# Optimization experiments

Measured on AMD Instinct MI355X. Metric: run time of the kernel, lower is better.

Reference implementation:

```python
import jax, jax.numpy as jnp
import numpy as np

B, L, D, H = 4, 2048, 256, 512


def silu_backward(x):
    s = jax.nn.silu(x)
    return s + jax.nn.sigmoid(x) * (1.0 - s)


def setup_inputs() -> dict:
    key = jax.random.key(0)
    ks = jax.random.split(key, 12)
    sc = 0.02
    return {
        "x": jax.random.normal(ks[0], (B, L, D), jnp.float32),
        "W1": jax.random.normal(ks[1], (B, H, D), jnp.float32) * sc,
        "W2": jax.random.normal(ks[2], (B, D, H), jnp.float32) * sc,
        "Wq": jax.random.normal(ks[3], (D, D), jnp.float32) * sc,
        "bq": jnp.zeros((D,), jnp.float32),
        "Wk": jax.random.normal(ks[4], (D, D), jnp.float32) * sc,
        "bk": jnp.zeros((D,), jnp.float32),
        "Wv": jax.random.normal(ks[5], (D, D), jnp.float32) * sc,
        "bv": jnp.zeros((D,), jnp.float32),
        "w_lr": jax.random.normal(ks[6], (D,), jnp.float32) * sc,
        "b_lr": jnp.zeros((), jnp.float32),
        "w_wd": jax.random.normal(ks[7], (D,), jnp.float32) * sc,
        "b_wd": jnp.zeros((), jnp.float32),
        "log_base_lr": jnp.asarray(np.log(0.1), jnp.float32),
        "log_base_wd": jnp.asarray(np.log(0.5), jnp.float32),
    }


def reference(x, W1, W2, Wq, bq, Wk, bk, Wv, bv, w_lr, b_lr, w_wd, b_wd, log_base_lr, log_base_wd):
    b, l, d = x.shape
    query = x @ Wq + bq
    key = x @ Wk + bk
    value = x @ Wv + bv
    lr = jnp.exp(log_base_lr) * jax.nn.sigmoid(x @ w_lr + b_lr)          # [b,l]
    log_wd = jnp.log(1.0 - jnp.exp(log_base_wd) * jax.nn.sigmoid(x @ w_wd + b_wd))  # [b,l]

    wd_cross = jnp.exp(jnp.cumsum(log_wd, axis=1))                       # [b,l]
    idx = jnp.arange(l)
    strict_upper = idx[:, None] < idx[None, :]                           # (m, j): j > m
    A = jnp.where(strict_upper[None], log_wd[:, None, :], 0.0)           # [b,m,j]
    wd_inner = jnp.exp(jnp.cumsum(A, axis=2)) * (idx[:, None] <= idx[None, :])[None]  # [b,m,j]

    X1 = key
    Z1 = jnp.einsum('bhd,bld->blh', W1, X1)
    X2 = jax.nn.silu(Z1)
    Z2 = jnp.einsum('bdh,blh->bld', W2, X2)
    grad_Z2 = Z2 - value
    grad_X2 = jnp.einsum('bdh,bld->blh', W2, grad_Z2)
    grad_Z1 = silu_backward(Z1) * grad_X2

    X1_ = query
    mask_X1X1_ = jnp.einsum('bld,bmd->blm', X1, X1_) * wd_inner
    Z1_inner = -jnp.einsum('blh,bl,blm->bmh', grad_Z1, lr, mask_X1X1_)
    Z1_cross = jnp.einsum('bhd,bld,bl->blh', W1, X1_, wd_cross)
    Z1_ = Z1_inner + Z1_cross

    W1_next = (-jnp.einsum('blh,bl,bld->bhd', grad_Z1, lr * wd_inner[:, :, -1], X1)
               + W1 * wd_cross[:, -1][:, None, None])

    X2_ = jax.nn.silu(Z1_)
    mask_X2X2_ = jnp.einsum('blh,bmh->blm', X2, X2_) * wd_inner
    Z2_inner = -jnp.einsum('bld,bl,blm->bmd', grad_Z2, lr, mask_X2X2_)
    Z2_cross = jnp.einsum('bdh,blh,bl->bld', W2, X2_, wd_cross)
    Z2_ = Z2_inner + Z2_cross

    W2_next = (-jnp.einsum('bld,bl,blh->bdh', grad_Z2, lr * wd_inner[:, :, -1], X2)
               + W2 * wd_cross[:, -1][:, None, None])

    return (Z2_, W1_next, W2_next)
```

## Files before the change

kernel.cpp:

```cpp
#include <hip/hip_runtime.h>

typedef __bf16 bf16;
typedef __bf16 bf16x8 __attribute__((ext_vector_type(8)));
typedef __bf16 bf16x4 __attribute__((ext_vector_type(4)));
typedef float  f32x4  __attribute__((ext_vector_type(4)));

#define SB 72
#define CUTOFF -18.0

__device__ __forceinline__ float silu_f(float x){
  float s = 1.f/(1.f+__expf(-x));
  return x*s;
}
__device__ __forceinline__ float silu_bwd_f(float x){
  float s = 1.f/(1.f+__expf(-x));
  float si = x*s;
  return si + s*(1.f-si);
}

struct MArgs {
  const bf16* A; const bf16* B;
  long sA, sB;
  int lda, ldb;
  int M, N, K;
  int mode;
  float* Cf; long sCf;
  bf16*  Cb; long sCb;
  bf16*  Cb2; long sCb2;
  bf16*  Ct;  long sCt;  int ldct;
  bf16*  Ct2; long sCt2;
  int ldc;
  const float* auxf; int ldax; long sAuxf;
  const bf16*  auxb; long sAuxb;
  const float* rowv; long sRowv;
  const float* rowv2; long sRowv2;
  const double* cd;  long sCd;
  const float* clp;  long sClp;
  bf16* Q; bf16* Ko; float* Vo; const float* bqkv;
};

template<int TM>
__device__ __forceinline__ void gemm_body(const MArgs& g, int bm, int bn, int bz)
{
  constexpr int TTP = (TM==64) ? 72 : 136;
  constexpr int BUF = (TM+64)*SB;
  __shared__ __align__(16) bf16 sh[2*BUF];

  const int row0 = bm*TM, col0 = bn*64;
  constexpr int NI  = TM/32;
  constexpr int TPR = 256/TM;
  constexpr int EPR = 64/TPR;
  constexpr int NCH = EPR/8;

  const bf16* A = g.A + (long)bz*g.sA;
  const bf16* B = g.B + (long)bz*g.sB;
  const double* cd = g.cd ? g.cd + (long)bz*g.sCd : (const double*)0;
  float* Cf = g.Cf ? g.Cf + (long)bz*g.sCf : (float*)0;
  bf16* Cb  = g.Cb ? g.Cb + (long)bz*g.sCb : (bf16*)0;
  bf16* Cb2 = g.Cb2 ? g.Cb2 + (long)bz*g.sCb2 : (bf16*)0;
  bf16* Ct  = g.Ct ? g.Ct + (long)bz*g.sCt : (bf16*)0;
  bf16* Ct2 = g.Ct2 ? g.Ct2 + (long)bz*g.sCt2 : (bf16*)0;
  const float* auxf = g.auxf ? g.auxf + (long)bz*g.sAuxf : (const float*)0;
  const bf16*  auxb = g.auxb ? g.auxb + (long)bz*g.sAuxb : (const bf16*)0;
  const float* rowv = g.rowv ? g.rowv + (long)bz*g.sRowv : (const float*)0;
  const float* rowv2 = g.rowv2 ? g.rowv2 + (long)bz*g.sRowv2 : (const float*)0;

  const int tid = threadIdx.x;
  const int mode = g.mode;
  const int lane = tid & 63;
  const int w = tid >> 6;
  const int wr = (w >> 1) * (TM/2), wc = (w & 1) * 32;
  const int l15 = lane & 15;
  const int quad = lane >> 4;

  f32x4 acc[NI][2];
  #pragma unroll
  for (int i=0;i<NI;i++)
    #pragma unroll
    for (int j=0;j<2;j++)
      #pragma unroll
      for (int r=0;r<4;r++) acc[i][j][r] = 0.f;

  const int rowA = tid / TPR, kA = (tid % TPR) * EPR;
  const int rowB = tid >> 2,  kB = (tid & 3) * 16;

  int klo = 0;
  if (cd) {
    const double cref = cd[g.K-1];
    const int nch = g.K >> 6;
    bool dead = (lane < nch-1) && ((cref - cd[lane*64+63]) < CUTOFF);
    unsigned long long mask = __ballot(dead);
    klo = (int)__builtin_ctzll(~mask) * 64;
  }

  const bf16* Abase = A + (long)(row0+rowA)*g.lda + kA;
  const bf16* Bbase = B + (long)(col0+rowB)*g.ldb + kB;

  bf16x8 paA[NCH], pbA0, pbA1, paB[NCH], pbB0, pbB1;
  #pragma unroll
  for (int p=0;p<NCH;p++) paA[p] = *(const bf16x8*)(Abase + klo + p*8);
  pbA0 = *(const bf16x8*)(Bbase + klo);
  pbA1 = *(const bf16x8*)(Bbase + klo + 8);
  if (klo + 64 < g.K) {
    #pragma unroll
    for (int p=0;p<NCH;p++) paB[p] = *(const bf16x8*)(Abase + klo + 64 + p*8);
    pbB0 = *(const bf16x8*)(Bbase + klo + 64);
    pbB1 = *(const bf16x8*)(Bbase + klo + 64 + 8);
  }

  auto compute = [&](const bf16* As, const bf16* Bs){
    #pragma unroll
    for (int ch=0; ch<2; ch++){
      bf16x8 af[NI], bf2[2];
      #pragma unroll
      for (int i=0;i<NI;i++) af[i]  = *(const bf16x8*)&As[(wr + i*16 + l15)*SB + ch*32 + quad*8];
      #pragma unroll
      for (int j=0;j<2;j++) bf2[j] = *(const bf16x8*)&Bs[(wc + j*16 + l15)*SB + ch*32 + quad*8];
      #pragma unroll
      for (int i=0;i<NI;i++)
        #pragma unroll
        for (int j=0;j<2;j++)
          acc[i][j] = __builtin_amdgcn_mfma_f32_16x16x32_bf16(af[i], bf2[j], acc[i][j], 0, 0, 0);
    }
  };

  for (int k0 = klo; k0 < g.K; k0 += 128) {
    {
      bf16* As = sh; bf16* Bs = sh + TM*SB;
      #pragma unroll
      for (int p=0;p<NCH;p++) *(bf16x8*)&As[rowA*SB + kA + p*8] = paA[p];
      *(bf16x8*)&Bs[rowB*SB + kB]     = pbA0;
      *(bf16x8*)&Bs[rowB*SB + kB + 8] = pbA1;
      __syncthreads();
      if (k0 + 128 < g.K) {
        #pragma unroll
        for (int p=0;p<NCH;p++) paA[p] = *(const bf16x8*)(Abase + k0 + 128 + p*8);
        pbA0 = *(const bf16x8*)(Bbase + k0 + 128);
        pbA1 = *(const bf16x8*)(Bbase + k0 + 128 + 8);
      }
      compute(As, Bs);
    }
    if (k0 + 64 < g.K) {
      bf16* As = sh + BUF; bf16* Bs = sh + BUF + TM*SB;
      #pragma unroll
      for (int p=0;p<NCH;p++) *(bf16x8*)&As[rowA*SB + kA + p*8] = paB[p];
      *(bf16x8*)&Bs[rowB*SB + kB]     = pbB0;
      *(bf16x8*)&Bs[rowB*SB + kB + 8] = pbB1;
      __syncthreads();
      if (k0 + 192 < g.K) {
        #pragma unroll
        for (int p=0;p<NCH;p++) paB[p] = *(const bf16x8*)(Abase + k0 + 192 + p*8);
        pbB0 = *(const bf16x8*)(Bbase + k0 + 192);
        pbB1 = *(const bf16x8*)(Bbase + k0 + 192 + 8);
      }
      compute(As, Bs);
    }
  }

  float clv = 0.f;
  if (mode == 10) clv = *(g.clp + (long)bz*g.sClp);

  const bool hasT = (TM==64) ? (mode==1 || mode==2 || mode==3)
                             : (mode==11 && col0 >= 256 && col0 < 512);

  #pragma unroll
  for (int i=0;i<NI;i++){
    const int rb = row0 + wr + i*16 + quad*4;
    const int rloc = wr + i*16 + quad*4;
    #pragma unroll
    for (int j=0;j<2;j++){
      const int c = col0 + wc + j*16 + l15;
      const int cloc = wc + j*16 + l15;
      bf16 tv[4], tv2[4]; bool doT = false, doT2 = false;
      #pragma unroll
      for (int reg=0; reg<4; reg++){
        const int r = rb + reg;
        float v = acc[i][j][reg];
        const long co = (long)r*g.ldc + c;
        switch (mode) {
          case 1: {
            Cb[co]  = (bf16)v;
            float sv = silu_f(v);
            Cb2[co] = (bf16)sv;
            tv[reg] = (bf16)(sv * rowv[r]); doT = true;
          } break;
          case 2: {
            bf16 o = (bf16)(v - auxf[(long)r*g.ldax + c]);
            Cb[co] = o; tv[reg] = o; doT = true;
          } break;
          case 3: {
            float v3 = silu_bwd_f((float)auxb[(long)r*g.ldax + c]) * v * rowv[r];
            tv[reg]  = (bf16)v3;
            tv2[reg] = (bf16)(v3 * rowv2[r]);
            doT = true; doT2 = true;
          } break;
          case 10: {
            Cf[co] = v + auxf[(long)r*g.ldax + c]*clv;
          } break;
          case 11: {
            float o = v + g.bqkv[c];
            if (c < 256)      g.Q [(long)r*256 + c]       = (bf16)o;
            else if (c < 512) { g.Ko[(long)r*256 + (c-256)] = (bf16)o; tv[reg] = (bf16)o; doT = true; }
            else              g.Vo[(long)r*256 + (c-512)] = o;
          } break;
        }
      }
      if (hasT && doT) {
        bf16x4 t4 = { tv[0], tv[1], tv[2], tv[3] };
        *(bf16x4*)&sh[cloc*TTP + rloc] = t4;
        if (doT2) {
          bf16x4 t4b = { tv2[0], tv2[1], tv2[2], tv2[3] };
          *(bf16x4*)&sh[64*72 + cloc*TTP + rloc] = t4b;
        }
      }
    }
  }

  if (hasT) {
    __syncthreads();
    if constexpr (TM == 64) {
      const int cl = tid >> 2, rl = (tid & 3)*16;
      bf16x8 u0 = *(const bf16x8*)&sh[cl*72 + rl];
      bf16x8 u1 = *(const bf16x8*)&sh[cl*72 + rl + 8];
      bf16* d = Ct + (long)(col0+cl)*g.ldct + row0 + rl;
      *(bf16x8*)d       = u0;
      *(bf16x8*)(d + 8) = u1;
      if (mode == 3) {
        bf16x8 v0 = *(const bf16x8*)&sh[64*72 + cl*72 + rl];
        bf16x8 v1 = *(const bf16x8*)&sh[64*72 + cl*72 + rl + 8];
        bf16* d2 = Ct2 + (long)(col0+cl)*g.ldct + row0 + rl;
        *(bf16x8*)d2       = v0;
        *(bf16x8*)(d2 + 8) = v1;
      }
    } else {
      const int cl = tid >> 2, rl = (tid & 3)*32;
      const int b = row0 / g.ldct, l0r = row0 % g.ldct;
      bf16* d = Ct + (long)b*g.sCt + (long)(col0-256+cl)*g.ldct + l0r + rl;
      #pragma unroll
      for (int p=0;p<4;p++)
        *(bf16x8*)(d + p*8) = *(const bf16x8*)&sh[cl*136 + rl + p*8];
    }
  }
}

__global__ __launch_bounds__(256)
void mfma_gemm128(MArgs g){ gemm_body<128>(g, blockIdx.x, blockIdx.y, blockIdx.z); }

__global__ __launch_bounds__(256)
void mfma_gemm64(MArgs g){ gemm_body<64>(g, blockIdx.x, blockIdx.y, blockIdx.z); }

__global__ __launch_bounds__(256)
void wnext_gemm(MArgs g1, MArgs g2){
  const int z = blockIdx.z;
  const MArgs& g = (z < 4) ? g1 : g2;
  const int bz = z & 3;
  if ((int)blockIdx.x*64 >= g.M || (int)blockIdx.y*64 >= g.N) return;
  gemm_body<64>(g, blockIdx.x, blockIdx.y, bz);
}

struct PArgs {
  const bf16 *A, *B1;
  long sA, sB1;
  const double* cd; long sCd;
  const float* lrv; long sLr;
  bf16* P;
};

template<int KS64, int ISLR>
__global__ __launch_bounds__(256)
void pgen(PArgs g)
{
  const int mt = blockIdx.x, slot = blockIdx.y, bz = blockIdx.z;
  const int m0 = mt*64;
  const int l0 = (m0 & ~127) - slot*128;
  if (l0 < 0) return;
  const double* cd = g.cd + (long)bz*g.sCd;
  const int lref = (l0+127 < m0) ? (l0+127) : m0;
  if (cd[m0] - cd[lref] < CUTOFF) return;

  const int K1 = KS64*64;
  const bf16* A  = g.A  + (long)bz*g.sA;
  const bf16* B1 = g.B1 + (long)bz*g.sB1;
  const float* lrv = ISLR ? (g.lrv + (long)bz*g.sLr) : (const float*)0;

  const int tid = threadIdx.x;
  const int lane = tid & 63, w = tid >> 6;
  const int wr = (w>>1)*32, wc = (w&1)*64;
  const int l15 = lane & 15, quad = lane >> 4;
  const int rowA = tid >> 2, kA = (tid & 3) * 16;
  const int rowB = tid >> 1, kB = (tid & 1) * 32;

  constexpr int BUFP = (64+128)*SB;
  __shared__ __align__(16) bf16 sh[2*BUFP];

  f32x4 O[2][4];
  #pragma unroll
  for (int i=0;i<2;i++)
    #pragma unroll
    for (int j=0;j<4;j++)
      #pragma unroll
      for (int r=0;r<4;r++) O[i][j][r] = 0.f;

  const bf16* Abase = A + (long)(m0+rowA)*K1 + kA;
  const bf16* Bbase = B1 + (long)(l0+rowB)*K1 + kB;

  bf16x8 paA0, paA1, pbA[4], paB0, paB1, pbB[4];
  paA0 = *(const bf16x8*)Abase;
  paA1 = *(const bf16x8*)(Abase + 8);
  #pragma unroll
  for (int p=0;p<4;p++) pbA[p] = *(const bf16x8*)(Bbase + p*8);
  paB0 = *(const bf16x8*)(Abase + 64);
  paB1 = *(const bf16x8*)(Abase + 64 + 8);
  #pragma unroll
  for (int p=0;p<4;p++) pbB[p] = *(const bf16x8*)(Bbase + 64 + p*8);

  auto compute = [&](const bf16* As, const bf16* Bs){
    #pragma unroll
    for (int ch=0; ch<2; ch++){
      bf16x8 af[2], bfr[4];
      #pragma unroll
      for (int i=0;i<2;i++) af[i]  = *(const bf16x8*)&As[(wr + i*16 + l15)*SB + ch*32 + quad*8];
      #pragma unroll
      for (int j=0;j<4;j++) bfr[j] = *(const bf16x8*)&Bs[(wc + j*16 + l15)*SB + ch*32 + quad*8];
      #pragma unroll
      for (int i=0;i<2;i++)
        #pragma unroll
        for (int j=0;j<4;j++)
          O[i][j] = __builtin_amdgcn_mfma_f32_16x16x32_bf16(af[i], bfr[j], O[i][j], 0, 0, 0);
    }
  };

  for (int ks=0; ks<KS64; ks+=2){
    {
      bf16* As = sh; bf16* Bs = sh + 64*SB;
      *(bf16x8*)&As[rowA*SB + kA]     = paA0;
      *(bf16x8*)&As[rowA*SB + kA + 8] = paA1;
      #pragma unroll
      for (int p=0;p<4;p++) *(bf16x8*)&Bs[rowB*SB + kB + p*8] = pbA[p];
      __syncthreads();
      if (ks+2 < KS64) {
        const int kn = (ks+2)*64;
        paA0 = *(const bf16x8*)(Abase + kn);
        paA1 = *(const bf16x8*)(Abase + kn + 8);
        #pragma unroll
        for (int p=0;p<4;p++) pbA[p] = *(const bf16x8*)(Bbase + kn + p*8);
      }
      compute(As, Bs);
    }
    {
      bf16* As = sh + BUFP; bf16* Bs = sh + BUFP + 64*SB;
      *(bf16x8*)&As[rowA*SB + kA]     = paB0;
      *(bf16x8*)&As[rowA*SB + kA + 8] = paB1;
      #pragma unroll
      for (int p=0;p<4;p++) *(bf16x8*)&Bs[rowB*SB + kB + p*8] = pbB[p];
      __syncthreads();
      if (ks+3 < KS64) {
        const int kn = (ks+3)*64;
        paB0 = *(const bf16x8*)(Abase + kn);
        paB1 = *(const bf16x8*)(Abase + kn + 8);
        #pragma unroll
        for (int p=0;p<4;p++) pbB[p] = *(const bf16x8*)(Bbase + kn + p*8);
      }
      compute(As, Bs);
    }
  }

  bf16* Pt = g.P + (((long)bz*32 + mt)*3 + slot) * (64*128);
  float cl[4], lv[4];
  #pragma unroll
  for (int j=0;j<4;j++){
    const int l = l0 + wc + j*16 + l15;
    cl[j] = (float)cd[l];
    if (ISLR) lv[j] = lrv[l];
  }
  #pragma unroll
  for (int i=0;i<2;i++)
    #pragma unroll
    for (int reg=0; reg<4; reg++){
      const int mloc = wr + i*16 + quad*4 + reg;
      const int m = m0 + mloc;
      const float cm = (float)cd[m];
      #pragma unroll
      for (int j=0;j<4;j++){
        const int lloc = wc + j*16 + l15;
        const int l = l0 + lloc;
        float v = -O[i][j][reg] * __expf(cm - cl[j]);
        if (ISLR) v *= lv[j];
        if (l > m) v = 0.f;
        Pt[mloc*128 + lloc] = (bf16)v;
      }
    }
}

struct CArgs {
  const bf16 *A, *W, *P, *B2;
  long sA, sW, sB2;
  int ldb2;
  const double* cd; long sCd;
  const float* wdc; long sWdc;
  float* Cf; long sCf;
  bf16* Cb; long sCb;
  int ldc;
};

template<int KS64, int SILU, int ZSPLIT>
__global__ __launch_bounds__(256)
void cons(CArgs g)
{
  const int mt = blockIdx.x;
  const int m0 = mt*64, n0 = blockIdx.y*64;
  const int bz   = ZSPLIT ? (blockIdx.z >> 1) : blockIdx.z;
  const int half = ZSPLIT ? (blockIdx.z & 1)  : 0;
  const int K1 = KS64*64;
  const bf16* A  = g.A  + (long)bz*g.sA;
  const bf16* W  = g.W  + (long)bz*g.sW;
  const bf16* B2 = g.B2 + (long)bz*g.sB2;
  const double* cd = g.cd + (long)bz*g.sCd;
  const float* wdc = g.wdc + (long)bz*g.sWdc;

  const int tid = threadIdx.x;
  const int lane = tid & 63, w = tid >> 6;
  const int wr = (w>>1)*32, wc = (w&1)*32;
  const int l15 = lane & 15, quad = lane >> 4;
  const int rowA = tid >> 2, kA = (tid & 3) * 16;

  bool alive[3];
  int nalive = 0;
  #pragma unroll
  for (int s=0;s<3;s++){
    const int l0 = (m0 & ~127) - s*128;
    bool a = (l0 >= 0);
    if (a) {
      const int lref = (l0+127 < m0) ? (l0+127) : m0;
      a = (cd[m0] - cd[lref] >= CUTOFF);
    }
    alive[s] = a; nalive += a ? 1 : 0;
  }
  if (ZSPLIT && half == 1 && nalive == 0) return;

  constexpr int BUFC = 128*SB;
  __shared__ __align__(16) bf16 sh[2*BUFC];

  f32x4 O[2][2];
  #pragma unroll
  for (int i=0;i<2;i++)
    #pragma unroll
    for (int j=0;j<2;j++)
      #pragma unroll
      for (int r=0;r<4;r++) O[i][j][r] = 0.f;

  auto compute = [&](const bf16* As, const bf16* Bs){
    #pragma unroll
    for (int ch=0; ch<2; ch++){
      bf16x8 af[2], bfr[2];
      #pragma unroll
      for (int i=0;i<2;i++) af[i]  = *(const bf16x8*)&As[(wr + i*16 + l15)*SB + ch*32 + quad*8];
      #pragma unroll
      for (int j=0;j<2;j++) bfr[j] = *(const bf16x8*)&Bs[(wc + j*16 + l15)*SB + ch*32 + quad*8];
      #pragma unroll
      for (int i=0;i<2;i++)
        #pragma unroll
        for (int j=0;j<2;j++)
          O[i][j] = __builtin_amdgcn_mfma_f32_16x16x32_bf16(af[i], bfr[j], O[i][j], 0, 0, 0);
    }
  };

  if (half == 0) {
    const bf16* Abase = A + (long)(m0+rowA)*K1 + kA;
    const bf16* Wbase = W + (long)(n0+rowA)*K1 + kA;
    bf16x8 aA0,aA1,wA0,wA1, aB0,aB1,wB0,wB1;
    aA0 = *(const bf16x8*)Abase;        aA1 = *(const bf16x8*)(Abase + 8);
    wA0 = *(const bf16x8*)Wbase;        wA1 = *(const bf16x8*)(Wbase + 8);
    aB0 = *(const bf16x8*)(Abase + 64); aB1 = *(const bf16x8*)(Abase + 72);
    wB0 = *(const bf16x8*)(Wbase + 64); wB1 = *(const bf16x8*)(Wbase + 72);
    for (int ks=0; ks<KS64; ks+=2){
      {
        bf16* As = sh; bf16* Bs = sh + 64*SB;
        *(bf16x8*)&As[rowA*SB + kA]     = aA0;
        *(bf16x8*)&As[rowA*SB + kA + 8] = aA1;
        *(bf16x8*)&Bs[rowA*SB + kA]     = wA0;
        *(bf16x8*)&Bs[rowA*SB + kA + 8] = wA1;
        __syncthreads();
        if (ks+2 < KS64) {
          const int kn = (ks+2)*64;
          aA0 = *(const bf16x8*)(Abase + kn); aA1 = *(const bf16x8*)(Abase + kn + 8);
          wA0 = *(const bf16x8*)(Wbase + kn); wA1 = *(const bf16x8*)(Wbase + kn + 8);
        }
        compute(As, Bs);
      }
      {
        bf16* As = sh + BUFC; bf16* Bs = sh + BUFC + 64*SB;
        *(bf16x8*)&As[rowA*SB + kA]     = aB0;
        *(bf16x8*)&As[rowA*SB + kA + 8] = aB1;
        *(bf16x8*)&Bs[rowA*SB + kA]     = wB0;
        *(bf16x8*)&Bs[rowA*SB + kA + 8] = wB1;
        __syncthreads();
        if (ks+3 < KS64) {
          const int kn = (ks+3)*64;
          aB0 = *(const bf16x8*)(Abase + kn); aB1 = *(const bf16x8*)(Abase + kn + 8);
          wB0 = *(const bf16x8*)(Wbase + kn); wB1 = *(const bf16x8*)(Wbase + kn + 8);
        }
        compute(As, Bs);
      }
    }
    #pragma unroll
    for (int i=0;i<2;i++)
      #pragma unroll
      for (int reg=0; reg<4; reg++){
        const float s = wdc[m0 + wr + i*16 + quad*4 + reg];
        #pragma unroll
        for (int j=0;j<2;j++) O[i][j][reg] *= s;
      }
  }

  if (!ZSPLIT || half == 1) {
    int s0a=0, s1a=0, s2a=0, na=0;
    #pragma unroll
    for (int s=0;s<3;s++) if (alive[s]) { if (na==0) s0a=s; else if (na==1) s1a=s; else s2a=s; na++; }
    const int nst = na*2;
    if (nst > 0) {
      auto Pptr = [&](int t)->const bf16* {
        const int i = t>>1;
        const int s = (i==0) ? s0a : ((i==1) ? s1a : s2a);
        return g.P + (((long)bz*32 + mt)*3 + s)*(64*128) + (long)rowA*128 + (t&1)*64 + kA;
      };
      auto Bptr = [&](int t)->const bf16* {
        const int i = t>>1;
        const int s = (i==0) ? s0a : ((i==1) ? s1a : s2a);
        const int l0 = (m0 & ~127) - s*128;
        return B2 + (long)(n0+rowA)*g.ldb2 + l0 + (t&1)*64 + kA;
      };
      bf16x8 pA0,pA1,bA0,bA1, pB0,pB1,bB0,bB1;
      { const bf16* pp = Pptr(0); pA0 = *(const bf16x8*)pp; pA1 = *(const bf16x8*)(pp+8);
        const bf16* bb = Bptr(0); bA0 = *(const bf16x8*)bb; bA1 = *(const bf16x8*)(bb+8); }
      { const bf16* pp = Pptr(1); pB0 = *(const bf16x8*)pp; pB1 = *(const bf16x8*)(pp+8);
        const bf16* bb = Bptr(1); bB0 = *(const bf16x8*)bb; bB1 = *(const bf16x8*)(bb+8); }
      for (int t=0; t<nst; t+=2){
        {
          bf16* As = sh; bf16* Bs = sh + 64*SB;
          *(bf16x8*)&As[rowA*SB + kA]     = pA0;
          *(bf16x8*)&As[rowA*SB + kA + 8] = pA1;
          *(bf16x8*)&Bs[rowA*SB + kA]     = bA0;
          *(bf16x8*)&Bs[rowA*SB + kA + 8] = bA1;
          __syncthreads();
          if (t+2 < nst) {
            const bf16* pp = Pptr(t+2); pA0 = *(const bf16x8*)pp; pA1 = *(const bf16x8*)(pp+8);
            const bf16* bb = Bptr(t+2); bA0 = *(const bf16x8*)bb; bA1 = *(const bf16x8*)(bb+8);
          }
          compute(As, Bs);
        }
        {
          bf16* As = sh + BUFC; bf16* Bs = sh + BUFC + 64*SB;
          *(bf16x8*)&As[rowA*SB + kA]     = pB0;
          *(bf16x8*)&As[rowA*SB + kA + 8] = pB1;
          *(bf16x8*)&Bs[rowA*SB + kA]     = bB0;
          *(bf16x8*)&Bs[rowA*SB + kA + 8] = bB1;
          __syncthreads();
          if (t+3 < nst) {
            const bf16* pp = Pptr(t+3); pB0 = *(const bf16x8*)pp; pB1 = *(const bf16x8*)(pp+8);
            const bf16* bb = Bptr(t+3); bB0 = *(const bf16x8*)bb; bB1 = *(const bf16x8*)(bb+8);
          }
          compute(As, Bs);
        }
      }
    }
  }

  #pragma unroll
  for (int i=0;i<2;i++){
    const int rb = m0 + wr + i*16 + quad*4;
    #pragma unroll
    for (int j=0;j<2;j++){
      const int c = n0 + wc + j*16 + l15;
      #pragma unroll
      for (int reg=0; reg<4; reg++){
        const long co = (long)(rb+reg)*g.ldc + c;
        if (ZSPLIT)     unsafeAtomicAdd(&g.Cf[(long)bz*g.sCf + co], O[i][j][reg]);
        else if (SILU)  g.Cb[(long)bz*g.sCb + co] = (bf16)silu_f(O[i][j][reg]);
        else            g.Cf[(long)bz*g.sCf + co] = O[i][j][reg];
      }
    }
  }
}

struct FrontArgs {
  const float *x, *W1, *W2, *Wq, *Wk, *Wv;
  bf16 *xb, *W1b, *W2b, *Wqkvt, *W2t;
  float* out0;
  const float *wlr, *blr, *wwd, *bwd, *lbl, *lbw;
  float *lr, *lw;
  long LD4, HD4, HD;
};

__global__ __launch_bounds__(256)
void front_kernel(FrontArgs f)
{
  __shared__ bf16 t[64][72];
  const int bid = blockIdx.x;
  const int tid = threadIdx.x;

  if (bid < 1536) {
    const float* src; bf16* dst; long n; long base;
    if (bid < 1024)      { src = f.x;  dst = f.xb;  n = f.LD4; base = (long)bid*2048; }
    else if (bid < 1280) { src = f.W1; dst = f.W1b; n = f.HD4; base = (long)(bid-1024)*2048; }
    else                 { src = f.W2; dst = f.W2b; n = f.HD4; base = (long)(bid-1280)*2048; }
    long i = base + (long)tid*8;
    if (i >= n) return;
    float4 a = *(const float4*)&src[i];
    float4 b = *(const float4*)&src[i+4];
    bf16x8 o;
    o[0]=(bf16)a.x; o[1]=(bf16)a.y; o[2]=(bf16)a.z; o[3]=(bf16)a.w;
    o[4]=(bf16)b.x; o[5]=(bf16)b.y; o[6]=(bf16)b.z; o[7]=(bf16)b.w;
    *(bf16x8*)&dst[i] = o;
    return;
  }
  if (bid < 2560) {
    long i = (long)(bid-1536)*2048 + (long)tid*8;
    float4 z = {0.f,0.f,0.f,0.f};
    *(float4*)&f.out0[i]   = z;
    *(float4*)&f.out0[i+4] = z;
    return;
  }
  if (bid < 2736) {
    const float* ip; bf16* op; int R, C; int r0, c0;
    if (bid < 2608) {
      const int r = bid - 2560;
      const int z = r >> 4, rem = r & 15;
      ip = z==0 ? f.Wq : (z==1 ? f.Wk : f.Wv);
      op = f.Wqkvt + (long)z*256*256;
      R = 256; C = 256;
      r0 = (rem & 3)*64; c0 = (rem >> 2)*64;
    } else {
      const int r = bid - 2608;
      const int b = r >> 5, rem = r & 31;
      ip = f.W2 + (long)b*f.HD;
      op = f.W2t + (long)b*f.HD;
      R = 256; C = 512;
      r0 = (rem & 3)*64; c0 = (rem >> 2)*64;
    }
    const int lr_ = tid>>2, lc = (tid&3)*16;
    #pragma unroll
    for (int q=0;q<4;q++){
      float4 a = *(const float4*)&ip[(long)(r0+lr_)*C + c0+lc + q*4];
      t[lr_][lc+q*4+0] = (bf16)a.x; t[lr_][lc+q*4+1] = (bf16)a.y;
      t[lr_][lc+q*4+2] = (bf16)a.z; t[lr_][lc+q*4+3] = (bf16)a.w;
    }
    __syncthreads();
    const int oc = tid>>2, orr = (tid&3)*16;
    bf16x8 u, v;
    #pragma unroll
    for (int i=0;i<8;i++){ u[i] = t[orr+i][oc]; v[i] = t[orr+8+i][oc]; }
    *(bf16x8*)&op[(long)(c0+oc)*R + r0+orr]   = u;
    *(bf16x8*)&op[(long)(c0+oc)*R + r0+orr+8] = v;
    return;
  }
  {
    const int row  = (bid-2736)*4 + (tid >> 6);
    const int lane = tid & 63;
    const float4 a = ((const float4*)(f.x + (long)row*256))[lane];
    const float4 u = ((const float4*)f.wlr)[lane];
    const float4 w = ((const float4*)f.wwd)[lane];
    float d1 = a.x*u.x + a.y*u.y + a.z*u.z + a.w*u.w;
    float d2 = a.x*w.x + a.y*w.y + a.z*w.z + a.w*w.w;
    #pragma unroll
    for (int off=32; off; off>>=1) {
      d1 += __shfl_down(d1, off);
      d2 += __shfl_down(d2, off);
    }
    if (lane == 0) {
      float s1 = 1.f/(1.f+expf(-(d1 + f.blr[0])));
      f.lr[row] = expf(f.lbl[0]) * s1;
      float s2 = 1.f/(1.f+expf(-(d2 + f.bwd[0])));
      f.lw[row] = logf(1.f - expf(f.lbw[0]) * s2);
    }
  }
}

__global__ __launch_bounds__(256)
void cumsum_kernel(const float* __restrict__ lw, const float* __restrict__ lr,
                   double* __restrict__ cd, float* __restrict__ wdc,
                   float* __restrict__ se1, float* __restrict__ se2, int L,
                   const float* __restrict__ bq, const float* __restrict__ bk,
                   const float* __restrict__ bv, float* __restrict__ bqkv)
{
  const int b = blockIdx.x;
  const int t = threadIdx.x;
  if (b == 4) {
    for (int i = t; i < 768; i += 256)
      bqkv[i] = (i<256) ? bq[i] : ((i<512) ? bk[i-256] : bv[i-512]);
    return;
  }
  const float* lwb = lw + (long)b*L;
  __shared__ double sum_s[256];
  double loc[8];
  double s = 0.0;
  #pragma unroll
  for (int i=0;i<8;i++){ s += (double)lwb[t*8+i]; loc[i] = s; }
  sum_s[t] = s;
  __syncthreads();
  for (int off=1; off<256; off<<=1){
    double v = 0.0;
    if (t >= off) v = sum_s[t-off];
    __syncthreads();
    sum_s[t] += v;
    __syncthreads();
  }
  const double prefix = (t > 0) ? sum_s[t-1] : 0.0;
  const double total  = sum_s[255];
  #pragma unroll
  for (int i=0;i<8;i++){
    double c = prefix + loc[i];
    long idx = (long)b*L + t*8 + i;
    cd[idx]  = c;
    wdc[idx] = (float)exp(c);
    double e = exp(total - c);
    se1[idx] = (float)(-e);
    se2[idx] = (float)(-e) * lr[idx];
  }
}

extern "C" void kernel_launch(void* const* d_in, const int* in_sizes, int n_in,
                              void* d_out, int out_size, void* d_ws, size_t ws_size,
                              hipStream_t stream)
{
  const int Bn = 4, L = 2048, D = 256, H = 512;
  const long LD = (long)L*D, LH = (long)L*H, HD = (long)H*D;

  const float* x   = (const float*)d_in[0];
  const float* W1  = (const float*)d_in[1];
  const float* W2  = (const float*)d_in[2];
  const float* Wq  = (const float*)d_in[3];
  const float* bq  = (const float*)d_in[4];
  const float* Wk  = (const float*)d_in[5];
  const float* bk  = (const float*)d_in[6];
  const float* Wv  = (const float*)d_in[7];
  const float* bv  = (const float*)d_in[8];
  const float* wlr = (const float*)d_in[9];
  const float* blr = (const float*)d_in[10];
  const float* wwd = (const float*)d_in[11];
  const float* bwd = (const float*)d_in[12];
  const float* lbl = (const float*)d_in[13];
  const float* lbw = (const float*)d_in[14];
  (void)in_sizes; (void)n_in; (void)out_size; (void)ws_size;

  float* out0 = (float*)d_out;
  float* out1 = out0 + (long)Bn*LD;
  float* out2 = out1 + (long)Bn*HD;

  char* wsp = (char*)d_ws;
  size_t off = 0;
  auto alloc = [&](size_t bytes)->void*{
    void* p = wsp + off; off += (bytes + 255) & ~(size_t)255; return p;
  };
  bf16* xb    = (bf16*)alloc((size_t)Bn*LD*2);
  bf16* Wqkvt = (bf16*)alloc((size_t)3*D*D*2);
  float* bqkv = (float*)alloc((size_t)3*D*4);
  bf16* W1b  = (bf16*)alloc((size_t)Bn*HD*2);
  bf16* W2b  = (bf16*)alloc((size_t)Bn*HD*2);
  bf16* W2t  = (bf16*)alloc((size_t)Bn*HD*2);
  bf16* Qb   = (bf16*)alloc((size_t)Bn*LD*2);
  bf16* Kb   = (bf16*)alloc((size_t)Bn*LD*2);
  bf16* Kt   = (bf16*)alloc((size_t)Bn*LD*2);
  float* Vf  = (float*)alloc((size_t)Bn*LD*4);
  bf16* Z1b  = (bf16*)alloc((size_t)Bn*LH*2);
  bf16* X2b  = (bf16*)alloc((size_t)Bn*LH*2);
  bf16* X2t  = (bf16*)alloc((size_t)Bn*LH*2);
  bf16* gZb  = (bf16*)alloc((size_t)Bn*LD*2);
  bf16* gZt  = (bf16*)alloc((size_t)Bn*LD*2);
  bf16* A1t  = (bf16*)alloc((size_t)Bn*LH*2);
  bf16* A1s  = (bf16*)alloc((size_t)Bn*LH*2);
  bf16* X2_b = (bf16*)alloc((size_t)Bn*LH*2);
  bf16* Pb1  = (bf16*)alloc((size_t)Bn*32*3*64*128*2);
  bf16* Pb2  = (bf16*)alloc((size_t)Bn*32*3*64*128*2);
  float* lrb = (float*)alloc((size_t)Bn*L*4);
  float* lwb = (float*)alloc((size_t)Bn*L*4);
  float* wdc = (float*)alloc((size_t)Bn*L*4);
  float* se1 = (float*)alloc((size_t)Bn*L*4);
  float* se2 = (float*)alloc((size_t)Bn*L*4);
  double* cdb = (double*)alloc((size_t)Bn*L*8);

  auto run128 = [&](const MArgs& g, int Z){
    dim3 grid(g.M/128, g.N/64, Z);
    mfma_gemm128<<<grid, 256, 0, stream>>>(g);
  };
  auto run64 = [&](const MArgs& g, int Z){
    dim3 grid(g.M/64, g.N/64, Z);
    mfma_gemm64<<<grid, 256, 0, stream>>>(g);
  };

  {
    FrontArgs f{};
    f.x = x; f.W1 = W1; f.W2 = W2; f.Wq = Wq; f.Wk = Wk; f.Wv = Wv;
    f.xb = xb; f.W1b = W1b; f.W2b = W2b; f.Wqkvt = Wqkvt; f.W2t = W2t;
    f.out0 = out0;
    f.wlr = wlr; f.blr = blr; f.wwd = wwd; f.bwd = bwd; f.lbl = lbl; f.lbw = lbw;
    f.lr = lrb; f.lw = lwb;
    f.LD4 = Bn*LD; f.HD4 = Bn*HD; f.HD = HD;
    front_kernel<<<dim3(4784), 256, 0, stream>>>(f);
  }
  cumsum_kernel<<<dim3(5), 256, 0, stream>>>(lwb, lrb, cdb, wdc, se1, se2, L, bq, bk, bv, bqkv);

  {
    MArgs g{}; g.A = xb; g.lda = D; g.B = Wqkvt; g.ldb = D;
    g.M = Bn*L; g.N = 3*D; g.K = D; g.mode = 11; g.ldc = 0;
    g.Q = Qb; g.Ko = Kb; g.Vo = Vf; g.bqkv = bqkv;
    g.Ct = Kt; g.sCt = LD; g.ldct = L;
    run128(g, 1);
  }
  {
    MArgs g{}; g.A = Kb; g.lda = D; g.sA = LD; g.B = W1b; g.ldb = D; g.sB = HD;
    g.M = L; g.N = H; g.K = D; g.mode = 1; g.ldc = H;
    g.Cb = Z1b; g.sCb = LH; g.Cb2 = X2b; g.sCb2 = LH;
    g.Ct = X2t; g.sCt = LH; g.ldct = L;
    g.rowv = se2; g.sRowv = L;
    run64(g, Bn);
  }
  {
    MArgs g{}; g.A = X2b; g.lda = H; g.sA = LH; g.B = W2b; g.ldb = H; g.sB = HD;
    g.M = L; g.N = D; g.K = H; g.mode = 2; g.ldc = D;
    g.auxf = Vf; g.ldax = D; g.sAuxf = LD; g.Cb = gZb; g.sCb = LD;
    g.Ct = gZt; g.sCt = LD; g.ldct = L; run64(g, Bn);
  }
  {
    MArgs g{}; g.A = gZb; g.lda = D; g.sA = LD; g.B = W2t; g.ldb = D; g.sB = HD;
    g.M = L; g.N = H; g.K = D; g.mode = 3; g.ldc = H;
    g.auxb = Z1b; g.ldax = H; g.sAuxb = LH;
    g.rowv = lrb; g.sRowv = L; g.rowv2 = se1; g.sRowv2 = L;
    g.Ct = A1t; g.sCt = LH; g.ldct = L;
    g.Ct2 = A1s; g.sCt2 = LH;
    run64(g, Bn);
  }
  {
    PArgs p{};
    p.A = Qb; p.sA = LD; p.B1 = Kb; p.sB1 = LD;
    p.cd = cdb; p.sCd = L; p.P = Pb1;
    pgen<4,0><<<dim3(32,3,Bn), 256, 0, stream>>>(p);
  }
  {
    CArgs c{};
    c.A = Qb; c.sA = LD; c.W = W1b; c.sW = HD;
    c.P = Pb1; c.B2 = A1t; c.sB2 = LH; c.ldb2 = L;
    c.cd = cdb; c.sCd = L; c.wdc = wdc; c.sWdc = L;
    c.Cb = X2_b; c.sCb = LH; c.ldc = H;
    cons<4,1,0><<<dim3(32, H/64, Bn), 256, 0, stream>>>(c);
  }
  {
    PArgs p{};
    p.A = X2_b; p.sA = LH; p.B1 = X2b; p.sB1 = LH;
    p.cd = cdb; p.sCd = L; p.lrv = lrb; p.sLr = L; p.P = Pb2;
    pgen<8,1><<<dim3(32,3,Bn), 256, 0, stream>>>(p);
  }
  {
    CArgs c{};
    c.A = X2_b; c.sA = LH; c.W = W2b; c.sW = HD;
    c.P = Pb2; c.B2 = gZt; c.sB2 = LD; c.ldb2 = L;
    c.cd = cdb; c.sCd = L; c.wdc = wdc; c.sWdc = L;
    c.Cf = out0; c.sCf = LD; c.ldc = D;
    cons<8,0,1><<<dim3(32, D/64, Bn*2), 256, 0, stream>>>(c);
  }
  {
    MArgs g1{}; g1.A = A1s; g1.lda = L; g1.sA = LH; g1.B = Kt; g1.ldb = L; g1.sB = LD;
    g1.M = H; g1.N = D; g1.K = L; g1.mode = 10; g1.ldc = D;
    g1.cd = cdb; g1.sCd = L;
    g1.auxf = W1; g1.ldax = D; g1.sAuxf = HD; g1.clp = wdc + (L-1); g1.sClp = L;
    g1.Cf = out1; g1.sCf = HD;

    MArgs g2{}; g2.A = gZt; g2.lda = L; g2.sA = LD; g2.B = X2t; g2.ldb = L; g2.sB = LH;
    g2.M = D; g2.N = H; g2.K = L; g2.mode = 10; g2.ldc = H;
    g2.cd = cdb; g2.sCd = L;
    g2.auxf = W2; g2.ldax = H; g2.sAuxf = HD; g2.clp = wdc + (L-1); g2.sClp = L;
    g2.Cf = out2; g2.sCf = HD;

    wnext_gemm<<<dim3(8,8,8), 256, 0, stream>>>(g1, g2);
  }
}
```

Measured before the change: 223.7 us.

## Fuse independent stages into combined launches and fold pgen into generic GEMM epilogue

```diff
diff --git a/kernel.cpp b/kernel.cpp
--- a/kernel.cpp
+++ b/kernel.cpp
@@ -85,7 +85,7 @@
   const int rowB = tid >> 2,  kB = (tid & 3) * 16;
 
   int klo = 0;
-  if (cd) {
+  if (cd && mode == 10) {
     const double cref = cd[g.K-1];
     const int nch = g.K >> 6;
     bool dead = (lane < nch-1) && ((cref - cd[lane*64+63]) < CUTOFF);
@@ -159,6 +159,14 @@
 
   float clv = 0.f;
   if (mode == 10) clv = *(g.clp + (long)bz*g.sClp);
+
+  bf16* Pt12 = (bf16*)0; int slotl0 = 0;
+  if (mode == 12) {
+    const int d = (row0 & ~127) - col0;
+    const int slot = (d + 64) >> 7;
+    slotl0 = (row0 & ~127) - slot*128;
+    Pt12 = Cb + ((long)bm*3 + slot) * (64*128);
+  }
 
   const bool hasT = (TM==64) ? (mode==1 || mode==2 || mode==3)
                              : (mode==11 && col0 >= 256 && col0 < 512);
@@ -203,6 +211,14 @@
             else if (c < 512) { g.Ko[(long)r*256 + (c-256)] = (bf16)o; tv[reg] = (bf16)o; doT = true; }
             else              g.Vo[(long)r*256 + (c-512)] = o;
           } break;
+          case 12: {
+            const float cm = (float)cd[r];
+            const float cl = (float)cd[c];
+            float pv = -v * __expf(cm - cl);
+            if (rowv) pv *= rowv[c];
+            if (c > r) pv = 0.f;
+            Pt12[(r - row0)*128 + (c - slotl0)] = (bf16)pv;
+          } break;
         }
       }
       if (hasT && doT) {
@@ -243,153 +259,117 @@
   }
 }
 
-__global__ __launch_bounds__(256)
-void mfma_gemm128(MArgs g){ gemm_body<128>(g, blockIdx.x, blockIdx.y, blockIdx.z); }
+__device__ __forceinline__ bool pgen_prep(const MArgs& g, int mt, int hs, int bz, int& bnOut)
+{
+  const int slot = hs >> 1, half = hs & 1;
+  const int m0 = mt*64;
+  const int l0 = (m0 & ~127) - slot*128;
+  if (l0 < 0) return false;
+  const double* cd = g.cd + (long)bz*g.sCd;
+  const int lref = (l0+127 < m0) ? (l0+127) : m0;
+  if (cd[m0] - cd[lref] < CUTOFF) return false;
+  const int l0h = l0 + half*64;
+  if (l0h > m0) {
+    bf16* Pt = g.Cb + (long)bz*g.sCb + ((long)mt*3 + slot) * (64*128);
+    const int row = threadIdx.x >> 2, colb = 64 + (threadIdx.x & 3)*16;
+    bf16x8 z;
+    #pragma unroll
+    for (int q=0;q<8;q++) z[q] = (bf16)0.f;
+    *(bf16x8*)&Pt[row*128 + colb]     = z;
+    *(bf16x8*)&Pt[row*128 + colb + 8] = z;
+    return false;
+  }
+  bnOut = l0h >> 6;
+  return true;
+}
 
 __global__ __launch_bounds__(256)
 void mfma_gemm64(MArgs g){ gemm_body<64>(g, blockIdx.x, blockIdx.y, blockIdx.z); }
 
+struct CumArgs {
+  const float* lw; const float* lr;
+  double* cd; float* wdc; float* se1; float* se2; int L;
+};
+
+__device__ __forceinline__ void cumsum_body(const CumArgs& a, int b)
+{
+  __shared__ double sum_s[256];
+  const int t = threadIdx.x;
+  const int L = a.L;
+  const float* lwb = a.lw + (long)b*L;
+  double loc[8];
+  double s = 0.0;
+  #pragma unroll
+  for (int i=0;i<8;i++){ s += (double)lwb[t*8+i]; loc[i] = s; }
+  sum_s[t] = s;
+  __syncthreads();
+  for (int off=1; off<256; off<<=1){
+    double v = 0.0;
+    if (t >= off) v = sum_s[t-off];
+    __syncthreads();
+    sum_s[t] += v;
+    __syncthreads();
+  }
+  const double prefix = (t > 0) ? sum_s[t-1] : 0.0;
+  const double total  = sum_s[255];
+  #pragma unroll
+  for (int i=0;i<8;i++){
+    double c = prefix + loc[i];
+    long idx = (long)b*L + t*8 + i;
+    a.cd[idx]  = c;
+    a.wdc[idx] = (float)exp(c);
+    double e = exp(total - c);
+    a.se1[idx] = (float)(-e);
+    a.se2[idx] = (float)(-e) * a.lr[idx];
+  }
+}
+
+
 __global__ __launch_bounds__(256)
-void wnext_gemm(MArgs g1, MArgs g2){
-  const int z = blockIdx.z;
-  const MArgs& g = (z < 4) ? g1 : g2;
-  const int bz = z & 3;
-  if ((int)blockIdx.x*64 >= g.M || (int)blockIdx.y*64 >= g.N) return;
-  gemm_body<64>(g, blockIdx.x, blockIdx.y, bz);
-}
-
-struct PArgs {
-  const bf16 *A, *B1;
-  long sA, sB1;
-  const double* cd; long sCd;
-  const float* lrv; long sLr;
-  bf16* P;
-};
-
-template<int KS64, int ISLR>
+void qkv_cum(MArgs g, CumArgs c)
+{
+  if (blockIdx.x == 64) {
+    if (blockIdx.y < 4) cumsum_body(c, blockIdx.y);
+    return;
+  }
+  gemm_body<128>(g, blockIdx.x, blockIdx.y, 0);
+}
+
 __global__ __launch_bounds__(256)
-void pgen(PArgs g)
+void gz2p1(MArgs gz, MArgs p1)
 {
-  const int mt = blockIdx.x, slot = blockIdx.y, bz = blockIdx.z;
-  const int m0 = mt*64;
-  const int l0 = (m0 & ~127) - slot*128;
-  if (l0 < 0) return;
-  const double* cd = g.cd + (long)bz*g.sCd;
-  const int lref = (l0+127 < m0) ? (l0+127) : m0;
-  if (cd[m0] - cd[lref] < CUTOFF) return;
-
-  const int K1 = KS64*64;
-  const bf16* A  = g.A  + (long)bz*g.sA;
-  const bf16* B1 = g.B1 + (long)bz*g.sB1;
-  const float* lrv = ISLR ? (g.lrv + (long)bz*g.sLr) : (const float*)0;
-
-  const int tid = threadIdx.x;
-  const int lane = tid & 63, w = tid >> 6;
-  const int wr = (w>>1)*32, wc = (w&1)*64;
-  const int l15 = lane & 15, quad = lane >> 4;
-  const int rowA = tid >> 2, kA = (tid & 3) * 16;
-  const int rowB = tid >> 1, kB = (tid & 1) * 32;
-
-  constexpr int BUFP = (64+128)*SB;
-  __shared__ __align__(16) bf16 sh[2*BUFP];
-
-  f32x4 O[2][4];
-  #pragma unroll
-  for (int i=0;i<2;i++)
-    #pragma unroll
-    for (int j=0;j<4;j++)
-      #pragma unroll
-      for (int r=0;r<4;r++) O[i][j][r] = 0.f;
-
-  const bf16* Abase = A + (long)(m0+rowA)*K1 + kA;
-  const bf16* Bbase = B1 + (long)(l0+rowB)*K1 + kB;
-
-  bf16x8 paA0, paA1, pbA[4], paB0, paB1, pbB[4];
-  paA0 = *(const bf16x8*)Abase;
-  paA1 = *(const bf16x8*)(Abase + 8);
-  #pragma unroll
-  for (int p=0;p<4;p++) pbA[p] = *(const bf16x8*)(Bbase + p*8);
-  paB0 = *(const bf16x8*)(Abase + 64);
-  paB1 = *(const bf16x8*)(Abase + 64 + 8);
-  #pragma unroll
-  for (int p=0;p<4;p++) pbB[p] = *(const bf16x8*)(Bbase + 64 + p*8);
-
-  auto compute = [&](const bf16* As, const bf16* Bs){
-    #pragma unroll
-    for (int ch=0; ch<2; ch++){
-      bf16x8 af[2], bfr[4];
-      #pragma unroll
-      for (int i=0;i<2;i++) af[i]  = *(const bf16x8*)&As[(wr + i*16 + l15)*SB + ch*32 + quad*8];
-      #pragma unroll
-      for (int j=0;j<4;j++) bfr[j] = *(const bf16x8*)&Bs[(wc + j*16 + l15)*SB + ch*32 + quad*8];
-      #pragma unroll
-      for (int i=0;i<2;i++)
-        #pragma unroll
-        for (int j=0;j<4;j++)
-          O[i][j] = __builtin_amdgcn_mfma_f32_16x16x32_bf16(af[i], bfr[j], O[i][j], 0, 0, 0);
-    }
-  };
-
-  for (int ks=0; ks<KS64; ks+=2){
-    {
-      bf16* As = sh; bf16* Bs = sh + 64*SB;
-      *(bf16x8*)&As[rowA*SB + kA]     = paA0;
-      *(bf16x8*)&As[rowA*SB + kA + 8] = paA1;
-      #pragma unroll
-      for (int p=0;p<4;p++) *(bf16x8*)&Bs[rowB*SB + kB + p*8] = pbA[p];
-      __syncthreads();
-      if (ks+2 < KS64) {
-        const int kn = (ks+2)*64;
-        paA0 = *(const bf16x8*)(Abase + kn);
-        paA1 = *(const bf16x8*)(Abase + kn + 8);
-        #pragma unroll
-        for (int p=0;p<4;p++) pbA[p] = *(const bf16x8*)(Bbase + kn + p*8);
-      }
-      compute(As, Bs);
-    }
-    {
-      bf16* As = sh + BUFP; bf16* Bs = sh + BUFP + 64*SB;
-      *(bf16x8*)&As[rowA*SB + kA]     = paB0;
-      *(bf16x8*)&As[rowA*SB + kA + 8] = paB1;
-      #pragma unroll
-      for (int p=0;p<4;p++) *(bf16x8*)&Bs[rowB*SB + kB + p*8] = pbB[p];
-      __syncthreads();
-      if (ks+3 < KS64) {
-        const int kn = (ks+3)*64;
-        paB0 = *(const bf16x8*)(Abase + kn);
-        paB1 = *(const bf16x8*)(Abase + kn + 8);
-        #pragma unroll
-        for (int p=0;p<4;p++) pbB[p] = *(const bf16x8*)(Bbase + kn + p*8);
-      }
-      compute(As, Bs);
-    }
-  }
-
-  bf16* Pt = g.P + (((long)bz*32 + mt)*3 + slot) * (64*128);
-  float cl[4], lv[4];
-  #pragma unroll
-  for (int j=0;j<4;j++){
-    const int l = l0 + wc + j*16 + l15;
-    cl[j] = (float)cd[l];
-    if (ISLR) lv[j] = lrv[l];
-  }
-  #pragma unroll
-  for (int i=0;i<2;i++)
-    #pragma unroll
-    for (int reg=0; reg<4; reg++){
-      const int mloc = wr + i*16 + quad*4 + reg;
-      const int m = m0 + mloc;
-      const float cm = (float)cd[m];
-      #pragma unroll
-      for (int j=0;j<4;j++){
-        const int lloc = wc + j*16 + l15;
-        const int l = l0 + lloc;
-        float v = -O[i][j][reg] * __expf(cm - cl[j]);
-        if (ISLR) v *= lv[j];
-        if (l > m) v = 0.f;
-        Pt[mloc*128 + lloc] = (bf16)v;
-      }
-    }
+  const int bid = blockIdx.x;
+  if (bid < 512) {
+    gemm_body<64>(gz, bid & 31, (bid >> 5) & 3, bid >> 7);
+    return;
+  }
+  const int i = bid - 512;
+  const int mt = i & 31, q = i >> 5;
+  const int hs = q % 6, bz = q / 6;
+  int bn;
+  if (pgen_prep(p1, mt, hs, bz, bn))
+    gemm_body<64>(p1, mt, bn, bz);
+}
+
+__global__ __launch_bounds__(256)
+void p2wn(MArgs p2, MArgs w1n, MArgs w2n)
+{
+  const int bid = blockIdx.x;
+  if (bid < 768) {
+    const int mt = bid & 31, q = bid >> 5;
+    const int hs = q % 6, bz = q / 6;
+    int bn;
+    if (pgen_prep(p2, mt, hs, bz, bn))
+      gemm_body<64>(p2, mt, bn, bz);
+    return;
+  }
+  const int i = bid - 768;
+  if (i < 128) {
+    gemm_body<64>(w1n, i & 7, (i >> 3) & 3, i >> 5);
+    return;
+  }
+  const int j = i - 128;
+  gemm_body<64>(w2n, j & 3, (j >> 2) & 7, j >> 5);
 }
 
 struct CArgs {
@@ -589,6 +569,7 @@
   float* out0;
   const float *wlr, *blr, *wwd, *bwd, *lbl, *lbw;
   float *lr, *lw;
+  const float *bq, *bk, *bv; float* bqkv;
   long LD4, HD4, HD;
 };
 
@@ -654,7 +635,7 @@
     *(bf16x8*)&op[(long)(c0+oc)*R + r0+orr+8] = v;
     return;
   }
-  {
+  if (bid < 4784) {
     const int row  = (bid-2736)*4 + (tid >> 6);
     const int lane = tid & 63;
     const float4 a = ((const float4*)(f.x + (long)row*256))[lane];
@@ -673,50 +654,10 @@
       float s2 = 1.f/(1.f+expf(-(d2 + f.bwd[0])));
       f.lw[row] = logf(1.f - expf(f.lbw[0]) * s2);
     }
-  }
-}
-
-__global__ __launch_bounds__(256)
-void cumsum_kernel(const float* __restrict__ lw, const float* __restrict__ lr,
-                   double* __restrict__ cd, float* __restrict__ wdc,
-                   float* __restrict__ se1, float* __restrict__ se2, int L,
-                   const float* __restrict__ bq, const float* __restrict__ bk,
-                   const float* __restrict__ bv, float* __restrict__ bqkv)
-{
-  const int b = blockIdx.x;
-  const int t = threadIdx.x;
-  if (b == 4) {
-    for (int i = t; i < 768; i += 256)
-      bqkv[i] = (i<256) ? bq[i] : ((i<512) ? bk[i-256] : bv[i-512]);
     return;
   }
-  const float* lwb = lw + (long)b*L;
-  __shared__ double sum_s[256];
-  double loc[8];
-  double s = 0.0;
-  #pragma unroll
-  for (int i=0;i<8;i++){ s += (double)lwb[t*8+i]; loc[i] = s; }
-  sum_s[t] = s;
-  __syncthreads();
-  for (int off=1; off<256; off<<=1){
-    double v = 0.0;
-    if (t >= off) v = sum_s[t-off];
-    __syncthreads();
-    sum_s[t] += v;
-    __syncthreads();
-  }
-  const double prefix = (t > 0) ? sum_s[t-1] : 0.0;
-  const double total  = sum_s[255];
-  #pragma unroll
-  for (int i=0;i<8;i++){
-    double c = prefix + loc[i];
-    long idx = (long)b*L + t*8 + i;
-    cd[idx]  = c;
-    wdc[idx] = (float)exp(c);
-    double e = exp(total - c);
-    se1[idx] = (float)(-e);
-    se2[idx] = (float)(-e) * lr[idx];
-  }
+  for (int i = tid; i < 768; i += 256)
+    f.bqkv[i] = (i<256) ? f.bq[i] : ((i<512) ? f.bk[i-256] : f.bv[i-512]);
 }
 
 extern "C" void kernel_launch(void* const* d_in, const int* in_sizes, int n_in,
@@ -779,14 +720,7 @@
   float* se2 = (float*)alloc((size_t)Bn*L*4);
   double* cdb = (double*)alloc((size_t)Bn*L*8);
 
-  auto run128 = [&](const MArgs& g, int Z){
-    dim3 grid(g.M/128, g.N/64, Z);
-    mfma_gemm128<<<grid, 256, 0, stream>>>(g);
-  };
-  auto run64 = [&](const MArgs& g, int Z){
-    dim3 grid(g.M/64, g.N/64, Z);
-    mfma_gemm64<<<grid, 256, 0, stream>>>(g);
-  };
+  const long sP = (long)32*3*64*128;
 
   {
     FrontArgs f{};
@@ -795,17 +729,17 @@
     f.out0 = out0;
     f.wlr = wlr; f.blr = blr; f.wwd = wwd; f.bwd = bwd; f.lbl = lbl; f.lbw = lbw;
     f.lr = lrb; f.lw = lwb;
+    f.bq = bq; f.bk = bk; f.bv = bv; f.bqkv = bqkv;
     f.LD4 = Bn*LD; f.HD4 = Bn*HD; f.HD = HD;
-    front_kernel<<<dim3(4784), 256, 0, stream>>>(f);
-  }
-  cumsum_kernel<<<dim3(5), 256, 0, stream>>>(lwb, lrb, cdb, wdc, se1, se2, L, bq, bk, bv, bqkv);
-
+    front_kernel<<<dim3(4785), 256, 0, stream>>>(f);
+  }
   {
     MArgs g{}; g.A = xb; g.lda = D; g.B = Wqkvt; g.ldb = D;
     g.M = Bn*L; g.N = 3*D; g.K = D; g.mode = 11; g.ldc = 0;
     g.Q = Qb; g.Ko = Kb; g.Vo = Vf; g.bqkv = bqkv;
     g.Ct = Kt; g.sCt = LD; g.ldct = L;
-    run128(g, 1);
+    CumArgs ca{ lwb, lrb, cdb, wdc, se1, se2, L };
+    qkv_cum<<<dim3(65, 12), 256, 0, stream>>>(g, ca);
   }
   {
     MArgs g{}; g.A = Kb; g.lda = D; g.sA = LD; g.B = W1b; g.ldb = D; g.sB = HD;
@@ -813,13 +747,20 @@
     g.Cb = Z1b; g.sCb = LH; g.Cb2 = X2b; g.sCb2 = LH;
     g.Ct = X2t; g.sCt = LH; g.ldct = L;
     g.rowv = se2; g.sRowv = L;
-    run64(g, Bn);
+    mfma_gemm64<<<dim3(32, 8, 4), 256, 0, stream>>>(g);
   }
   {
-    MArgs g{}; g.A = X2b; g.lda = H; g.sA = LH; g.B = W2b; g.ldb = H; g.sB = HD;
-    g.M = L; g.N = D; g.K = H; g.mode = 2; g.ldc = D;
-    g.auxf = Vf; g.ldax = D; g.sAuxf = LD; g.Cb = gZb; g.sCb = LD;
-    g.Ct = gZt; g.sCt = LD; g.ldct = L; run64(g, Bn);
+    MArgs gz{}; gz.A = X2b; gz.lda = H; gz.sA = LH; gz.B = W2b; gz.ldb = H; gz.sB = HD;
+    gz.M = L; gz.N = D; gz.K = H; gz.mode = 2; gz.ldc = D;
+    gz.auxf = Vf; gz.ldax = D; gz.sAuxf = LD; gz.Cb = gZb; gz.sCb = LD;
+    gz.Ct = gZt; gz.sCt = LD; gz.ldct = L;
+
+    MArgs p1{}; p1.A = Qb; p1.lda = D; p1.sA = LD; p1.B = Kb; p1.ldb = D; p1.sB = LD;
+    p1.K = D; p1.mode = 12; p1.ldc = 0;
+    p1.Cb = Pb1; p1.sCb = sP;
+    p1.cd = cdb; p1.sCd = L;
+
+    gz2p1<<<dim3(512 + 768), 256, 0, stream>>>(gz, p1);
   }
   {
     MArgs g{}; g.A = gZb; g.lda = D; g.sA = LD; g.B = W2t; g.ldb = D; g.sB = HD;
@@ -828,13 +769,7 @@
     g.rowv = lrb; g.sRowv = L; g.rowv2 = se1; g.sRowv2 = L;
     g.Ct = A1t; g.sCt = LH; g.ldct = L;
     g.Ct2 = A1s; g.sCt2 = LH;
-    run64(g, Bn);
-  }
-  {
-    PArgs p{};
-    p.A = Qb; p.sA = LD; p.B1 = Kb; p.sB1 = LD;
-    p.cd = cdb; p.sCd = L; p.P = Pb1;
-    pgen<4,0><<<dim3(32,3,Bn), 256, 0, stream>>>(p);
+    mfma_gemm64<<<dim3(32, 8, 4), 256, 0, stream>>>(g);
   }
   {
     CArgs c{};
@@ -845,10 +780,25 @@
     cons<4,1,0><<<dim3(32, H/64, Bn), 256, 0, stream>>>(c);
   }
   {
-    PArgs p{};
-    p.A = X2_b; p.sA = LH; p.B1 = X2b; p.sB1 = LH;
-    p.cd = cdb; p.sCd = L; p.lrv = lrb; p.sLr = L; p.P = Pb2;
-    pgen<8,1><<<dim3(32,3,Bn), 256, 0, stream>>>(p);
+    MArgs p2{}; p2.A = X2_b; p2.lda = H; p2.sA = LH; p2.B = X2b; p2.ldb = H; p2.sB = LH;
+    p2.K = H; p2.mode = 12; p2.ldc = 0;
+    p2.Cb = Pb2; p2.sCb = sP;
+    p2.cd = cdb; p2.sCd = L;
+    p2.rowv = lrb; p2.sRowv = L;
+
+    MArgs g1{}; g1.A = A1s; g1.lda = L; g1.sA = LH; g1.B = Kt; g1.ldb = L; g1.sB = LD;
+    g1.M = H; g1.N = D; g1.K = L; g1.mode = 10; g1.ldc = D;
+    g1.cd = cdb; g1.sCd = L;
+    g1.auxf = W1; g1.ldax = D; g1.sAuxf = HD; g1.clp = wdc + (L-1); g1.sClp = L;
+    g1.Cf = out1; g1.sCf = HD;
+
+    MArgs g2{}; g2.A = gZt; g2.lda = L; g2.sA = LD; g2.B = X2t; g2.ldb = L; g2.sB = LH;
+    g2.M = D; g2.N = H; g2.K = L; g2.mode = 10; g2.ldc = H;
+    g2.cd = cdb; g2.sCd = L;
+    g2.auxf = W2; g2.ldax = H; g2.sAuxf = HD; g2.clp = wdc + (L-1); g2.sClp = L;
+    g2.Cf = out2; g2.sCf = HD;
+
+    p2wn<<<dim3(768 + 128 + 128), 256, 0, stream>>>(p2, g1, g2);
   }
   {
     CArgs c{};
@@ -858,19 +808,4 @@
     c.Cf = out0; c.sCf = LD; c.ldc = D;
     cons<8,0,1><<<dim3(32, D/64, Bn*2), 256, 0, stream>>>(c);
   }
-  {
-    MArgs g1{}; g1.A = A1s; g1.lda = L; g1.sA = LH; g1.B = Kt; g1.ldb = L; g1.sB = LD;
-    g1.M = H; g1.N = D; g1.K = L; g1.mode = 10; g1.ldc = D;
-    g1.cd = cdb; g1.sCd = L;
-    g1.auxf = W1; g1.ldax = D; g1.sAuxf = HD; g1.clp = wdc + (L-1); g1.sClp = L;
-    g1.Cf = out1; g1.sCf = HD;
-
-    MArgs g2{}; g2.A = gZt; g2.lda = L; g2.sA = LD; g2.B = X2t; g2.ldb = L; g2.sB = LH;
-    g2.M = D; g2.N = H; g2.K = L; g2.mode = 10; g2.ldc = H;
-    g2.cd = cdb; g2.sCd = L;
-    g2.auxf = W2; g2.ldax = H; g2.sAuxf = HD; g2.clp = wdc + (L-1); g2.sClp = L;
-    g2.Cf = out2; g2.sCf = HD;
-
-    wnext_gemm<<<dim3(8,8,8), 256, 0, stream>>>(g1, g2);
-  }
-}
+}
```

Measured after the change: 255.4 us. 14.2% more time.
